# Performance work log

Hardware: AMD Instinct MI355X
Metric: run time of the kernel (lower is better)

## Reference

```python
import jax, jax.numpy as jnp
import numpy as np

MARGIN = 0.4

def setup_inputs() -> dict:
    key = jax.random.key(0)
    k1, k2, k3 = jax.random.split(key, 3)
    D = 128
    N = 500000
    return {
        "anchor": jax.random.normal(k1, (1, D), dtype=jnp.float32),
        "positive": jax.random.normal(k2, (1, D), dtype=jnp.float32),
        "negatives": jax.random.normal(k3, (N, D), dtype=jnp.float32),
    }

def reference(anchor, positive, negatives):
    # cosine branch of TripletLoss:
    # distance[i] = dot(anchor[0], positive[0]) - dot(anchor[0], negatives[i]) + margin
    # losses = relu(distance); return losses.mean()  (size_average=True default)
    a = anchor[0]                      # [D]
    pos_sim = jnp.dot(a, positive[0])  # scalar
    neg_sim = negatives @ a            # [N]  fused matvec replaces the python loop
    losses = jax.nn.relu(pos_sim - neg_sim + MARGIN)
    return jnp.mean(losses)
```

## Files before the change

### kernel.cpp

```cpp
#include <hip/hip_runtime.h>

#define MARGIN 0.4f

__global__ __launch_bounds__(256) void triplet_loss_kernel(
    const float* __restrict__ anchor,
    const float* __restrict__ positive,
    const float* __restrict__ negatives,
    float* __restrict__ out, int N)
{
    const int lane = threadIdx.x & 63;
    const int waveInBlock = threadIdx.x >> 6;

    float ps = anchor[lane] * positive[lane] + anchor[lane + 64] * positive[lane + 64];
    #pragma unroll
    for (int m = 1; m < 64; m <<= 1)
        ps += __shfl_xor(ps, m, 64);
    const float c = ps + MARGIN;

    const int col = (lane & 31) << 2;
    const float4 af = *reinterpret_cast<const float4*>(anchor + col);

    const int half = lane >> 5;
    const long long nPairs = (long long)N >> 1;
    long long p = (long long)blockIdx.x * 4 + waveInBlock;
    const long long stride = (long long)gridDim.x * 4;

    float acc = 0.0f;
    for (; p < nPairs; p += stride) {
        const long long row = 2 * p + half;
        const float4 nf = *reinterpret_cast<const float4*>(negatives + row * 128 + col);
        float d = nf.x * af.x + nf.y * af.y + nf.z * af.z + nf.w * af.w;
        d += __shfl_xor(d, 1, 64);
        d += __shfl_xor(d, 2, 64);
        d += __shfl_xor(d, 4, 64);
        d += __shfl_xor(d, 8, 64);
        d += __shfl_xor(d, 16, 64);
        if ((lane & 31) == 0) {
            const float loss = c - d;
            acc += loss > 0.0f ? loss : 0.0f;
        }
    }

    if ((N & 1) && blockIdx.x == 0 && waveInBlock == 0) {
        const long long row = (long long)N - 1;
        if (half == 0) {
            const float4 nf = *reinterpret_cast<const float4*>(negatives + row * 128 + col);
            float d = nf.x * af.x + nf.y * af.y + nf.z * af.z + nf.w * af.w;
            d += __shfl_xor(d, 1, 64);
            d += __shfl_xor(d, 2, 64);
            d += __shfl_xor(d, 4, 64);
            d += __shfl_xor(d, 8, 64);
            d += __shfl_xor(d, 16, 64);
            if (lane == 0) {
                const float loss = c - d;
                acc += loss > 0.0f ? loss : 0.0f;
            }
        }
    }

    #pragma unroll
    for (int m = 1; m < 64; m <<= 1)
        acc += __shfl_xor(acc, m, 64);

    __shared__ float waveSums[4];
    if (lane == 0) waveSums[waveInBlock] = acc;
    __syncthreads();
    if (threadIdx.x == 0) {
        const float s = waveSums[0] + waveSums[1] + waveSums[2] + waveSums[3];
        atomicAdd(out, s * (1.0f / (float)N));
    }
}

extern "C" void kernel_launch(void* const* d_in, const int* in_sizes, int n_in,
                              void* d_out, int out_size, void* d_ws, size_t ws_size,
                              hipStream_t stream) {
    const float* anchor    = (const float*)d_in[0];
    const float* positive  = (const float*)d_in[1];
    const float* negatives = (const float*)d_in[2];
    float* out = (float*)d_out;

    const int D = 128;
    const int N = in_sizes[2] / D;

    hipMemsetAsync(out, 0, sizeof(float), stream);

    triplet_loss_kernel<<<2048, 256, 0, stream>>>(anchor, positive, negatives, out, N);
}
```

Measured before the change: 350.2 us.

## Assign one negative row per thread instead of half-wavefront per row

Replaces the grid-stride loop, where 32 lanes cooperatively load one row and reduce it with shuffles, with a one-row-per-thread mapping over a grid sized to N. The anchor is staged in shared memory and each thread streams its 512-byte row as float4 loads into four accumulators. This removes the per-row shuffle reductions but makes neighbouring lanes read addresses 512 bytes apart, so global loads are no longer coalesced. It also launches about 2000 blocks that each issue one atomicAdd, and every thread recomputes the positive dot product serially.

```diff
diff --git a/kernel.cpp b/kernel.cpp
--- a/kernel.cpp
+++ b/kernel.cpp
@@ -2,70 +2,55 @@
 
 #define MARGIN 0.4f
 
-__global__ __launch_bounds__(256) void triplet_loss_kernel(
+__global__ __launch_bounds__(256) void triplet_row_kernel(
     const float* __restrict__ anchor,
     const float* __restrict__ positive,
     const float* __restrict__ negatives,
     float* __restrict__ out, int N)
 {
-    const int lane = threadIdx.x & 63;
-    const int waveInBlock = threadIdx.x >> 6;
+    __shared__ float s_a[128];
+    __shared__ float waveSums[4];
 
-    float ps = anchor[lane] * positive[lane] + anchor[lane + 64] * positive[lane + 64];
+    const int tid = threadIdx.x;
+    if (tid < 128) s_a[tid] = anchor[tid];
+    __syncthreads();
+
+    float ps = 0.0f;
     #pragma unroll
-    for (int m = 1; m < 64; m <<= 1)
-        ps += __shfl_xor(ps, m, 64);
+    for (int j = 0; j < 128; ++j)
+        ps = fmaf(anchor[j], positive[j], ps);
     const float c = ps + MARGIN;
 
-    const int col = (lane & 31) << 2;
-    const float4 af = *reinterpret_cast<const float4*>(anchor + col);
+    const float4* s_a4 = reinterpret_cast<const float4*>(s_a);
 
-    const int half = lane >> 5;
-    const long long nPairs = (long long)N >> 1;
-    long long p = (long long)blockIdx.x * 4 + waveInBlock;
-    const long long stride = (long long)gridDim.x * 4;
-
+    const int row = blockIdx.x * 256 + tid;
     float acc = 0.0f;
-    for (; p < nPairs; p += stride) {
-        const long long row = 2 * p + half;
-        const float4 nf = *reinterpret_cast<const float4*>(negatives + row * 128 + col);
-        float d = nf.x * af.x + nf.y * af.y + nf.z * af.z + nf.w * af.w;
-        d += __shfl_xor(d, 1, 64);
-        d += __shfl_xor(d, 2, 64);
-        d += __shfl_xor(d, 4, 64);
-        d += __shfl_xor(d, 8, 64);
-        d += __shfl_xor(d, 16, 64);
-        if ((lane & 31) == 0) {
-            const float loss = c - d;
-            acc += loss > 0.0f ? loss : 0.0f;
+    if (row < N) {
+        const float4* rp = reinterpret_cast<const float4*>(negatives + (size_t)row * 128);
+        float d0 = 0.0f, d1 = 0.0f, d2 = 0.0f, d3 = 0.0f;
+        #pragma unroll
+        for (int j = 0; j < 32; ++j) {
+            const float4 n = rp[j];
+            const float4 a = s_a4[j];
+            d0 = fmaf(n.x, a.x, d0);
+            d1 = fmaf(n.y, a.y, d1);
+            d2 = fmaf(n.z, a.z, d2);
+            d3 = fmaf(n.w, a.w, d3);
         }
-    }
-
-    if ((N & 1) && blockIdx.x == 0 && waveInBlock == 0) {
-        const long long row = (long long)N - 1;
-        if (half == 0) {
-            const float4 nf = *reinterpret_cast<const float4*>(negatives + row * 128 + col);
-            float d = nf.x * af.x + nf.y * af.y + nf.z * af.z + nf.w * af.w;
-            d += __shfl_xor(d, 1, 64);
-            d += __shfl_xor(d, 2, 64);
-            d += __shfl_xor(d, 4, 64);
-            d += __shfl_xor(d, 8, 64);
-            d += __shfl_xor(d, 16, 64);
-            if (lane == 0) {
-                const float loss = c - d;
-                acc += loss > 0.0f ? loss : 0.0f;
-            }
-        }
+        const float dot = (d0 + d1) + (d2 + d3);
+        const float loss = c - dot;
+        acc = loss > 0.0f ? loss : 0.0f;
     }
 
     #pragma unroll
     for (int m = 1; m < 64; m <<= 1)
         acc += __shfl_xor(acc, m, 64);
 
-    __shared__ float waveSums[4];
+    const int lane = tid & 63;
+    const int waveInBlock = tid >> 6;
     if (lane == 0) waveSums[waveInBlock] = acc;
     __syncthreads();
-    if (threadIdx.x == 0) {
+    if (tid == 0) {
         const float s = waveSums[0] + waveSums[1] + waveSums[2] + waveSums[3];
         atomicAdd(out, s * (1.0f / (float)N));
     }
@@ -84,5 +69,6 @@
 
     hipMemsetAsync(out, 0, sizeof(float), stream);
 
-    triplet_loss_kernel<<<2048, 256, 0, stream>>>(anchor, positive, negatives, out, N);
+    const int blocks = (N + 255) / 256;
+    triplet_row_kernel<<<blocks, 256, 0, stream>>>(anchor, positive, negatives, out, N);
 }
```

Result: slower. 358.4 us (+2.3%).
